# Optimization experiments

Hardware: AMD Instinct MI355X
Metric: run time of the kernel (lower is better)

The kernel has to match this reference:

```python
import jax, jax.numpy as jnp
import numpy as np

E, D, H, T = 16, 1024, 4096, 8192  # num_expert, d_model, d_hidden (4h), total tokens


def setup_inputs() -> dict:
    key = jax.random.key(0)
    k0, k1, k2, k3, k4 = jax.random.split(key, 5)
    inp = jax.random.normal(k0, (T, D), dtype=jnp.float32)
    # FMoELinear init: kaiming-uniform-like, bound = 1/sqrt(fan_in)
    s1 = 1.0 / np.sqrt(D)
    s2 = 1.0 / np.sqrt(H)
    w1 = jax.random.uniform(k1, (E, H, D), jnp.float32, -s1, s1)  # htoh4 weight [E, out, in]
    b1 = jax.random.uniform(k2, (E, H), jnp.float32, -s1, s1)
    w2 = jax.random.uniform(k3, (E, D, H), jnp.float32, -s2, s2)  # h4toh weight
    b2 = jax.random.uniform(k4, (E, D), jnp.float32, -s2, s2)
    fwd_expert_count = jnp.full((E,), T // E, dtype=jnp.int32)  # tokens per expert (sums to T)
    return dict(inp=inp, w1=w1, b1=b1, w2=w2, b2=b2, fwd_expert_count=fwd_expert_count)


def reference(inp, w1, b1, w2, b2, fwd_expert_count):
    # Grouped GEMM: tokens are sorted by expert; segment e gets expert e's FFN.
    counts = np.asarray(fwd_expert_count)          # static per-expert row counts
    offs = np.concatenate([[0], np.cumsum(counts)])
    outs = []
    for e in range(counts.shape[0]):               # loop over fixed small expert set
        seg = inp[offs[e]:offs[e + 1]]             # [n_e, D]
        h = seg @ w1[e].T + b1[e]                  # htoh4: [n_e, H]
        h = jax.nn.gelu(h, approximate=False)      # torch F.gelu default (exact)
        outs.append(h @ w2[e].T + b2[e])           # h4toh: [n_e, D]
    return jnp.concatenate(outs, axis=0)           # [T, D]
```

## Files before the change

kernel.cpp:

```cpp
#include <hip/hip_runtime.h>
#include <hip/hip_bf16.h>

typedef float f32x4 __attribute__((ext_vector_type(4)));
typedef __bf16 bf16x8 __attribute__((ext_vector_type(8)));
typedef unsigned short u16;
typedef unsigned short u16x4 __attribute__((ext_vector_type(4)));
typedef unsigned short u16x8 __attribute__((ext_vector_type(8)));

#define BM 128
#define BN 128
#define BK 32
#define NT 256

__device__ __forceinline__ u16 f2bf(float f) {
  unsigned u = __builtin_bit_cast(unsigned, f);
  u += 0x7fffu + ((u >> 16) & 1u);
  return (u16)(u >> 16);
}

template<bool A_BF16, bool DO_GELU, bool OUT_BF16>
__global__ __launch_bounds__(NT)
void ffn_gemm(const void* __restrict__ Ain, const float* __restrict__ Bw,
              const float* __restrict__ bias, void* __restrict__ Out,
              const int* __restrict__ counts, int E, int T, int N, int K)
{
  int mt = blockIdx.y;
  int row0 = 0, cnt = 0, e = 0;
  for (; e < E; ++e) {
    cnt = counts[e];
    int nt = (cnt + BM - 1) / BM;
    if (mt < nt) break;
    mt -= nt; row0 += cnt;
  }
  if (e >= E) return;
  int valid = cnt - mt * BM; if (valid > BM) valid = BM;
  row0 += mt * BM;
  const int n0 = blockIdx.x * BN;

  const float* Be = Bw + (long long)e * N * K;
  const float* be = bias + (long long)e * N;

  __shared__ u16 As[2][BM][BK];
  __shared__ u16 Bs[2][BN][BK];

  const int t = threadIdx.x;
  const int lane = t & 63;
  const int w = t >> 6, wr = w >> 1, wc = w & 1;

  f32x4 acc[4][4];
#pragma unroll
  for (int i = 0; i < 4; ++i)
#pragma unroll
    for (int j = 0; j < 4; ++j) acc[i][j] = (f32x4){0.f, 0.f, 0.f, 0.f};

  const int NKT = K / BK;

  float rA[16]; u16x8 rAu[2]; float rB[16];

  auto load_tile = [&](int kt) {
    const int k0 = kt * BK;
    if constexpr (!A_BF16) {
      const float* Af = (const float*)Ain;
#pragma unroll
      for (int i = 0; i < 4; ++i) {
        int c = i * NT + t;
        int row = c >> 3, col = (c & 7) << 2;
        int gr = row0 + row; if (gr > T - 1) gr = T - 1;
        f32x4 v = *(const f32x4*)(Af + (long long)gr * K + k0 + col);
        rA[i*4+0] = v[0]; rA[i*4+1] = v[1]; rA[i*4+2] = v[2]; rA[i*4+3] = v[3];
      }
    } else {
      const u16* Ab = (const u16*)Ain;
#pragma unroll
      for (int i = 0; i < 2; ++i) {
        int c = i * NT + t;
        int row = c >> 2, col = (c & 3) << 3;
        int gr = row0 + row; if (gr > T - 1) gr = T - 1;
        rAu[i] = *(const u16x8*)(Ab + (long long)gr * K + k0 + col);
      }
    }
#pragma unroll
    for (int i = 0; i < 4; ++i) {
      int c = i * NT + t;
      int row = c >> 3, col = (c & 7) << 2;
      f32x4 v = *(const f32x4*)(Be + (long long)(n0 + row) * K + k0 + col);
      rB[i*4+0] = v[0]; rB[i*4+1] = v[1]; rB[i*4+2] = v[2]; rB[i*4+3] = v[3];
    }
  };

  auto store_tile = [&](int buf) {
    if constexpr (!A_BF16) {
#pragma unroll
      for (int i = 0; i < 4; ++i) {
        int c = i * NT + t;
        int row = c >> 3, col = (c & 7) << 2;
        int kg = (col >> 3) ^ ((row >> 1) & 3);
        int off = kg * 8 + ((col >> 2) & 1) * 4;
        u16x4 pk = { f2bf(rA[i*4+0]), f2bf(rA[i*4+1]), f2bf(rA[i*4+2]), f2bf(rA[i*4+3]) };
        *(u16x4*)&As[buf][row][off] = pk;
      }
    } else {
#pragma unroll
      for (int i = 0; i < 2; ++i) {
        int c = i * NT + t;
        int row = c >> 2, col = (c & 3) << 3;
        int kg = (col >> 3) ^ ((row >> 1) & 3);
        *(u16x8*)&As[buf][row][kg * 8] = rAu[i];
      }
    }
#pragma unroll
    for (int i = 0; i < 4; ++i) {
      int c = i * NT + t;
      int row = c >> 3, col = (c & 7) << 2;
      int kg = (col >> 3) ^ ((row >> 1) & 3);
      int off = kg * 8 + ((col >> 2) & 1) * 4;
      u16x4 pk = { f2bf(rB[i*4+0]), f2bf(rB[i*4+1]), f2bf(rB[i*4+2]), f2bf(rB[i*4+3]) };
      *(u16x4*)&Bs[buf][row][off] = pk;
    }
  };

  load_tile(0);
  store_tile(0);
  __syncthreads();

  for (int kt = 0; kt < NKT; ++kt) {
    const int cur = kt & 1;
    if (kt + 1 < NKT) load_tile(kt + 1);

    bf16x8 af[4], bfr[4];
    const int rl = lane & 15;
    const int kg = (lane >> 4) ^ ((rl >> 1) & 3);
#pragma unroll
    for (int mf = 0; mf < 4; ++mf)
      af[mf] = __builtin_bit_cast(bf16x8, *(const u16x8*)&As[cur][wr*64 + mf*16 + rl][kg*8]);
#pragma unroll
    for (int nf = 0; nf < 4; ++nf)
      bfr[nf] = __builtin_bit_cast(bf16x8, *(const u16x8*)&Bs[cur][wc*64 + nf*16 + rl][kg*8]);
#pragma unroll
    for (int mf = 0; mf < 4; ++mf)
#pragma unroll
      for (int nf = 0; nf < 4; ++nf)
        acc[mf][nf] = __builtin_amdgcn_mfma_f32_16x16x32_bf16(af[mf], bfr[nf], acc[mf][nf], 0, 0, 0);

    if (kt + 1 < NKT) {
      store_tile(cur ^ 1);
      __syncthreads();
    }
  }

  const int cl = lane & 15, rg = lane >> 4;
#pragma unroll
  for (int mf = 0; mf < 4; ++mf) {
#pragma unroll
    for (int nf = 0; nf < 4; ++nf) {
      int gcol = n0 + wc*64 + nf*16 + cl;
      float bv = be[gcol];
#pragma unroll
      for (int r = 0; r < 4; ++r) {
        int lrow = wr*64 + mf*16 + rg*4 + r;
        if (lrow < valid) {
          float v = acc[mf][nf][r] + bv;
          if constexpr (DO_GELU)
            v = 0.5f * v * (1.0f + erff(v * 0.70710678118654752f));
          long long idx = (long long)(row0 + lrow) * N + gcol;
          if constexpr (OUT_BF16) ((u16*)Out)[idx] = f2bf(v);
          else                    ((float*)Out)[idx] = v;
        }
      }
    }
  }
}

extern "C" void kernel_launch(void* const* d_in, const int* in_sizes, int n_in,
                              void* d_out, int out_size, void* d_ws, size_t ws_size,
                              hipStream_t stream) {
  const float* inp = (const float*)d_in[0];
  const float* w1  = (const float*)d_in[1];
  const float* b1  = (const float*)d_in[2];
  const float* w2  = (const float*)d_in[3];
  const float* b2  = (const float*)d_in[4];
  const int* cnts  = (const int*)d_in[5];

  const int E = in_sizes[5];
  const int H = in_sizes[2] / E;
  const int D = in_sizes[4] / E;
  const int T = in_sizes[0] / D;

  u16* hbuf = (u16*)d_ws;

  const int tiles = (T + BM - 1) / BM + E;
  dim3 blk(NT);

  dim3 g1(H / BN, tiles);
  ffn_gemm<false, true, true><<<g1, blk, 0, stream>>>(
      (const void*)inp, w1, b1, (void*)hbuf, cnts, E, T, H, D);

  dim3 g2(D / BN, tiles);
  ffn_gemm<true, false, false><<<g2, blk, 0, stream>>>(
      (const void*)hbuf, w2, b2, d_out, cnts, E, T, D, H);
}
```

Measured before the change: 342.2 us.

## Remap workgroups per XCD, deepen global-load prefetch, precompute load offsets

The grid is flattened to 1D, and block indices are remapped so that consecutive tiles land on the same XCD, which is meant to improve L2 reuse of the weight and activation tiles. Global loads are now issued two K-steps ahead, and the LDS store for the next buffer is placed before the MFMA block, so memory latency overlaps more compute. Per-thread global offsets are hoisted out of the K loop. The cost is higher register pressure from holding an extra prefetched tile, plus a remap that assumes the x dimension is a power of two.

```diff
diff --git a/kernel.cpp b/kernel.cpp
--- a/kernel.cpp
+++ b/kernel.cpp
@@ -22,20 +22,28 @@
 __global__ __launch_bounds__(NT)
 void ffn_gemm(const void* __restrict__ Ain, const float* __restrict__ Bw,
               const float* __restrict__ bias, void* __restrict__ Out,
-              const int* __restrict__ counts, int E, int T, int N, int K)
+              const int* __restrict__ counts, int E, int T, int N, int K,
+              int gxl, int nwg)
 {
-  int mt = blockIdx.y;
+  int flat = blockIdx.x;
+  {
+    int q = nwg >> 3, r = nwg & 7;
+    int xcd = flat & 7, idx = flat >> 3;
+    flat = (xcd < r ? xcd * (q + 1) : r * (q + 1) + (xcd - r) * q) + idx;
+  }
+  int mt = flat >> gxl;
+  const int n0 = (flat & ((1 << gxl) - 1)) * BN;
+
   int row0 = 0, cnt = 0, e = 0;
   for (; e < E; ++e) {
     cnt = counts[e];
-    int nt = (cnt + BM - 1) / BM;
-    if (mt < nt) break;
-    mt -= nt; row0 += cnt;
+    int ntl = (cnt + BM - 1) / BM;
+    if (mt < ntl) break;
+    mt -= ntl; row0 += cnt;
   }
   if (e >= E) return;
   int valid = cnt - mt * BM; if (valid > BM) valid = BM;
   row0 += mt * BM;
-  const int n0 = blockIdx.x * BN;
 
   const float* Be = Bw + (long long)e * N * K;
   const float* be = bias + (long long)e * N;
@@ -55,35 +63,52 @@
 
   const int NKT = K / BK;
 
+  long long offA[4];
+  if constexpr (!A_BF16) {
+#pragma unroll
+    for (int i = 0; i < 4; ++i) {
+      int c = i * NT + t;
+      int row = c >> 3, col = (c & 7) << 2;
+      int gr = row0 + row; if (gr > T - 1) gr = T - 1;
+      offA[i] = (long long)gr * K + col;
+    }
+  } else {
+#pragma unroll
+    for (int i = 0; i < 2; ++i) {
+      int c = i * NT + t;
+      int row = c >> 2, col = (c & 3) << 3;
+      int gr = row0 + row; if (gr > T - 1) gr = T - 1;
+      offA[i] = (long long)gr * K + col;
+    }
+  }
+  long long offB[4];
+#pragma unroll
+  for (int i = 0; i < 4; ++i) {
+    int c = i * NT + t;
+    int row = c >> 3, col = (c & 7) << 2;
+    offB[i] = (long long)(n0 + row) * K + col;
+  }
+
   float rA[16]; u16x8 rAu[2]; float rB[16];
 
-  auto load_tile = [&](int kt) {
+  auto load_g = [&](int kt) {
     const int k0 = kt * BK;
     if constexpr (!A_BF16) {
       const float* Af = (const float*)Ain;
 #pragma unroll
       for (int i = 0; i < 4; ++i) {
-        int c = i * NT + t;
-        int row = c >> 3, col = (c & 7) << 2;
-        int gr = row0 + row; if (gr > T - 1) gr = T - 1;
-        f32x4 v = *(const f32x4*)(Af + (long long)gr * K + k0 + col);
+        f32x4 v = *(const f32x4*)(Af + offA[i] + k0);
         rA[i*4+0] = v[0]; rA[i*4+1] = v[1]; rA[i*4+2] = v[2]; rA[i*4+3] = v[3];
       }
     } else {
       const u16* Ab = (const u16*)Ain;
 #pragma unroll
-      for (int i = 0; i < 2; ++i) {
-        int c = i * NT + t;
-        int row = c >> 2, col = (c & 3) << 3;
-        int gr = row0 + row; if (gr > T - 1) gr = T - 1;
-        rAu[i] = *(const u16x8*)(Ab + (long long)gr * K + k0 + col);
-      }
+      for (int i = 0; i < 2; ++i)
+        rAu[i] = *(const u16x8*)(Ab + offA[i] + k0);
     }
 #pragma unroll
     for (int i = 0; i < 4; ++i) {
-      int c = i * NT + t;
-      int row = c >> 3, col = (c & 7) << 2;
-      f32x4 v = *(const f32x4*)(Be + (long long)(n0 + row) * K + k0 + col);
+      f32x4 v = *(const f32x4*)(Be + offB[i] + k0);
       rB[i*4+0] = v[0]; rB[i*4+1] = v[1]; rB[i*4+2] = v[2]; rB[i*4+3] = v[3];
     }
   };
@@ -119,13 +144,13 @@
     }
   };
 
-  load_tile(0);
+  load_g(0);
   store_tile(0);
+  load_g(1);
   __syncthreads();
 
   for (int kt = 0; kt < NKT; ++kt) {
     const int cur = kt & 1;
-    if (kt + 1 < NKT) load_tile(kt + 1);
 
     bf16x8 af[4], bfr[4];
     const int rl = lane & 15;
@@ -136,16 +161,17 @@
 #pragma unroll
     for (int nf = 0; nf < 4; ++nf)
       bfr[nf] = __builtin_bit_cast(bf16x8, *(const u16x8*)&Bs[cur][wc*64 + nf*16 + rl][kg*8]);
+
+    if (kt + 1 < NKT) store_tile(cur ^ 1);
+    if (kt + 2 < NKT) load_g(kt + 2);
+
 #pragma unroll
     for (int mf = 0; mf < 4; ++mf)
 #pragma unroll
       for (int nf = 0; nf < 4; ++nf)
         acc[mf][nf] = __builtin_amdgcn_mfma_f32_16x16x32_bf16(af[mf], bfr[nf], acc[mf][nf], 0, 0, 0);
 
-    if (kt + 1 < NKT) {
-      store_tile(cur ^ 1);
-      __syncthreads();
-    }
+    if (kt + 1 < NKT) __syncthreads();
   }
 
   const int cl = lane & 15, rg = lane >> 4;
@@ -191,11 +217,13 @@
   const int tiles = (T + BM - 1) / BM + E;
   dim3 blk(NT);
 
-  dim3 g1(H / BN, tiles);
-  ffn_gemm<false, true, true><<<g1, blk, 0, stream>>>(
-      (const void*)inp, w1, b1, (void*)hbuf, cnts, E, T, H, D);
-
-  dim3 g2(D / BN, tiles);
-  ffn_gemm<true, false, false><<<g2, blk, 0, stream>>>(
-      (const void*)hbuf, w2, b2, d_out, cnts, E, T, D, H);
+  const int gx1 = H / BN, gxl1 = __builtin_ctz(gx1);
+  const int nwg1 = gx1 * tiles;
+  ffn_gemm<false, true, true><<<dim3(nwg1), blk, 0, stream>>>(
+      (const void*)inp, w1, b1, (void*)hbuf, cnts, E, T, H, D, gxl1, nwg1);
+
+  const int gx2 = D / BN, gxl2 = __builtin_ctz(gx2);
+  const int nwg2 = gx2 * tiles;
+  ffn_gemm<true, false, false><<<dim3(nwg2), blk, 0, stream>>>(
+      (const void*)hbuf, w2, b2, d_out, cnts, E, T, D, H, gxl2, nwg2);
 }
```

Measured after the change: 414.6 us. 1.21x slower.
